# Kernel optimization log

Measured on AMD Instinct MI355X. Metric: run time of the kernel, lower is better.

## Reference

```python
import jax, jax.numpy as jnp
import numpy as np

D_MODEL = 1024
N_HEADS = 16
D_K = D_MODEL // N_HEADS


def setup_inputs() -> dict:
    key = jax.random.key(0)
    ks = jax.random.split(key, 12)
    B, S, D, H = 2, 2048, D_MODEL, N_HEADS
    s = 1.0 / np.sqrt(D)
    inp = {
        "x": jax.random.normal(ks[0], (B, S, D), jnp.float32),
        "Wq": jax.random.normal(ks[1], (D, D), jnp.float32) * s,
        "bq": jnp.zeros((D,), jnp.float32),
        "Wk": jax.random.normal(ks[2], (D, D), jnp.float32) * s,
        "bk": jnp.zeros((D,), jnp.float32),
        "Wv": jax.random.normal(ks[3], (D, D), jnp.float32) * s,
        "bv": jnp.zeros((D,), jnp.float32),
        "Wo": jax.random.normal(ks[4], (D, D), jnp.float32) * s,
        "bo": jnp.zeros((D,), jnp.float32),
        "Wp": jax.random.normal(ks[5], (D, H), jnp.float32) * s,
        "bp": jnp.zeros((H,), jnp.float32),
        "alpha": jax.random.normal(ks[6], (H,), jnp.float32) * 0.1,
    }
    return inp


def reference(x, Wq, bq, Wk, bk, Wv, bv, Wo, bo, Wp, bp, alpha):
    B, S, D = x.shape
    H, dk = N_HEADS, D_K
    scale = dk ** -0.5
    # projections -> (B, H, S, dk)
    Q = (x @ Wq + bq).reshape(B, S, H, dk).transpose(0, 2, 1, 3)
    K = (x @ Wk + bk).reshape(B, S, H, dk).transpose(0, 2, 1, 3)
    V = (x @ Wv + bv).reshape(B, S, H, dk).transpose(0, 2, 1, 3)
    scores = jnp.einsum("bhid,bhjd->bhij", Q, K) * scale  # (B,H,S,S)
    # phase derived from x: (B,S,H) -> (B,H,S)
    phase = (x @ Wp + bp).transpose(0, 2, 1)
    # coherence(i,j) = cos(phi_i - phi_j), per batch/head
    coherence = jnp.cos(phase[:, :, :, None] - phase[:, :, None, :])
    scores = scores + alpha[None, :, None, None] * coherence
    attn = jax.nn.softmax(scores, axis=-1)
    out = jnp.einsum("bhij,bhjd->bhid", attn, V)  # (B,H,S,dk)
    out = out.transpose(0, 2, 1, 3).reshape(B, S, D)
    return out @ Wo + bo
```

## Files before the change

kernel.cpp:

```cpp
#include <hip/hip_runtime.h>
#include <math.h>


#define S_LEN 2048
#define NHEADS 16

typedef __attribute__((ext_vector_type(8))) short short8;
typedef __attribute__((ext_vector_type(4))) float floatx4;
typedef __attribute__((ext_vector_type(4))) unsigned int uintx4;

__device__ inline unsigned short f2bf(float f) {
    union { float f; unsigned int i; } v; v.f = f;
    unsigned int u = v.i;
    return (unsigned short)((u + 0x7fffu + ((u >> 16) & 1u)) >> 16);
}
__device__ inline unsigned int pack2_bf16(float hi, float lo) {
    union { float f; unsigned int u; } a, b; a.f = hi; b.f = lo;
    return __builtin_amdgcn_perm(a.u, b.u, 0x07060302u);
}
__device__ inline void async_copy16(const unsigned short* src, unsigned short* dst_lds) {
    __builtin_amdgcn_global_load_lds(
        (const __attribute__((address_space(1))) unsigned int*)(src),
        (__attribute__((address_space(3))) unsigned int*)(dst_lds), 16, 0, 0);
}
__device__ inline void async_copy4(const float* src, float* dst_lds) {
    __builtin_amdgcn_global_load_lds(
        (const __attribute__((address_space(1))) unsigned int*)(src),
        (__attribute__((address_space(3))) unsigned int*)(dst_lds), 4, 0, 0);
}

__global__ __launch_bounds__(256) void prep_kernel(
    const float* __restrict__ x, const float* __restrict__ Wp,
    const float* __restrict__ bp,
    const float* __restrict__ w0, const float* __restrict__ w1,
    const float* __restrict__ w2, const float* __restrict__ w3,
    unsigned short* __restrict__ d0, unsigned short* __restrict__ d1,
    unsigned short* __restrict__ d2, unsigned short* __restrict__ d3,
    float* __restrict__ cosP, float* __restrict__ sinP,
    unsigned short* __restrict__ xb) {
    __shared__ __align__(16) unsigned short shmem[64 * 72];
    int t = threadIdx.x;
    if (blockIdx.x < 4096) {
        float* red = reinterpret_cast<float*>(shmem);
        int bid = blockIdx.x;
        int b = bid >> 11, s = bid & 2047;
        int h = t & 15, c = t >> 4;
        const float* xr = x + (size_t)bid * 1024;
        {
            float4 xv = *reinterpret_cast<const float4*>(&xr[t * 4]);
            uint2 o;
            o.x = (unsigned int)f2bf(xv.x) | ((unsigned int)f2bf(xv.y) << 16);
            o.y = (unsigned int)f2bf(xv.z) | ((unsigned int)f2bf(xv.w) << 16);
            *reinterpret_cast<uint2*>(&xb[(size_t)bid * 1024 + t * 4]) = o;
        }
        float acc = 0.f;
#pragma unroll 8
        for (int kk = 0; kk < 64; kk++) {
            int k = c * 64 + kk;
            acc += xr[k] * Wp[k * 16 + h];
        }
        red[t] = acc;
        __syncthreads();
        if (t < 16) {
            float sum = 0.f;
#pragma unroll
            for (int c2 = 0; c2 < 16; c2++) sum += red[c2 * 16 + t];
            sum += bp[t];
            float sv, cv;
            __sincosf(sum, &sv, &cv);
            size_t o = ((size_t)b * NHEADS + t) * S_LEN + s;
            cosP[o] = cv; sinP[o] = sv;
        }
    } else {
        unsigned short (*tile)[72] = reinterpret_cast<unsigned short (*)[72]>(shmem);
        int bid = blockIdx.x - 4096;
        int mat = bid >> 8;
        int tl  = bid & 255;
        int tr = tl >> 4, tc = tl & 15;
        const float* src    = (mat == 0) ? w0 : (mat == 1) ? w1 : (mat == 2) ? w2 : w3;
        unsigned short* dst = (mat == 0) ? d0 : (mat == 1) ? d1 : (mat == 2) ? d2 : d3;
        int col = t & 63, rbase = (t >> 6) * 16;
#pragma unroll
        for (int i = 0; i < 16; i++) {
            int row = rbase + i;
            tile[row][col] = f2bf(src[(size_t)(tr * 64 + row) * 1024 + tc * 64 + col]);
        }
        __syncthreads();
#pragma unroll
        for (int i = 0; i < 16; i++) {
            int row = rbase + i;
            dst[(size_t)(tc * 64 + row) * 1024 + tr * 64 + col] = tile[col][row];
        }
    }
}

template <int MT>
__global__ __launch_bounds__(256) void gemm_bt(
    const unsigned short* __restrict__ A, const unsigned short* __restrict__ BT,
    int N, int mode,
    const float* __restrict__ b0, const float* __restrict__ b1,
    const float* __restrict__ b2,
    unsigned short* __restrict__ o0, unsigned short* __restrict__ o1,
    unsigned short* __restrict__ o2, float* __restrict__ of) {
    __shared__ __align__(16) unsigned short As[MT * 32];
    __shared__ __align__(16) unsigned short Bs[128 * 32];
    const int K = 1024;
    const int MI = MT / 32;
    int t = threadIdx.x;
    int mBase = blockIdx.x * MT;
    int nBase = blockIdx.y * 128;
    int w = t >> 6, lane = t & 63, l15 = lane & 15, quad = lane >> 4;
    int wm = (w & 1) * (MT / 2), wn = (w >> 1) * 64;
    floatx4 acc[MI][4];
#pragma unroll
    for (int i = 0; i < MI; i++)
#pragma unroll
        for (int j = 0; j < 4; j++) acc[i][j] = (floatx4){0.f, 0.f, 0.f, 0.f};

    int arow = t >> 2, aseg = (t & 3) * 8;
    for (int k0 = 0; k0 < K; k0 += 32) {
        __syncthreads();
#pragma unroll
        for (int i = 0; i < MT / 64; i++)
            async_copy16(&A[(size_t)(mBase + i * 64 + arow) * K + k0 + aseg],
                         &As[(i * 64 + arow) * 32 + aseg]);
#pragma unroll
        for (int i = 0; i < 2; i++)
            async_copy16(&BT[(size_t)(nBase + i * 64 + arow) * K + k0 + aseg],
                         &Bs[(i * 64 + arow) * 32 + aseg]);
        __syncthreads();
        short8 af[MI], bfr[4];
#pragma unroll
        for (int mi = 0; mi < MI; mi++)
            af[mi] = *reinterpret_cast<const short8*>(&As[(wm + mi * 16 + l15) * 32 + quad * 8]);
#pragma unroll
        for (int ni = 0; ni < 4; ni++)
            bfr[ni] = *reinterpret_cast<const short8*>(&Bs[(wn + ni * 16 + l15) * 32 + quad * 8]);
#pragma unroll
        for (int mi = 0; mi < MI; mi++)
#pragma unroll
            for (int ni = 0; ni < 4; ni++)
                acc[mi][ni] = __builtin_amdgcn_mfma_f32_16x16x32_bf16(af[mi], bfr[ni], acc[mi][ni], 0, 0, 0);
    }

#pragma unroll
    for (int mi = 0; mi < MI; mi++) {
        int rowB = mBase + wm + mi * 16 + quad * 4;
#pragma unroll
        for (int ni = 0; ni < 4; ni++) {
            int col = nBase + wn + ni * 16 + l15;
            if (mode == 0) {
                float bias = b0[col];
#pragma unroll
                for (int r = 0; r < 4; r++) {
                    of[(size_t)(rowB + r) * N + col] = acc[mi][ni][r] + bias;
                }
            } else {
                int mat = col >> 10, nn = col & 1023;
                int h = nn >> 6, d = nn & 63;
                int b = rowB >> 11, sidx = rowB & 2047;
                if (mat == 2) {
                    float bv = b2[nn];
                    int jj = sidx & 63;
                    int a2 = jj >> 5, c2 = (jj >> 4) & 1, bb = jj & 15;
                    size_t rowOff = ((size_t)((b * NHEADS + h) * 64 + d)) * S_LEN +
                                    (sidx & ~63) + a2 * 32 + c2;
#pragma unroll
                    for (int r = 0; r < 4; r++)
                        o2[rowOff + 2 * (bb + r)] = f2bf(acc[mi][ni][r] + bv);
                } else {
                    const float* bias  = (mat == 0) ? b0 : b1;
                    unsigned short* op = (mat == 0) ? o0 : o1;
                    float bv = bias[nn];
                    float scl = (mat == 0) ? 0.18033688f : 1.0f;
#pragma unroll
                    for (int r = 0; r < 4; r++) {
                        float cv = (acc[mi][ni][r] + bv) * scl;
                        op[(((size_t)b * NHEADS + h) * S_LEN + (sidx + r)) * 64 + d] = f2bf(cv);
                    }
                }
            }
        }
    }
}

__global__ __launch_bounds__(512) void attn_kernel(
    const unsigned short* __restrict__ Qg, const unsigned short* __restrict__ Kg,
    const unsigned short* __restrict__ VTg,
    const float* __restrict__ cosP, const float* __restrict__ sinP,
    const float* __restrict__ alpha, unsigned short* __restrict__ ctx) {
    __shared__ __align__(16) unsigned short KsB[2][64 * 64];
    __shared__ __align__(16) unsigned short VtB[2][64 * 64];
    __shared__ __align__(16) float csB[2][128];
    __shared__ __align__(16) unsigned short Plb[8][16 * 72];

    int bid = blockIdx.x;
    int bh = bid >> 4, qt = bid & 15;
    int t = threadIdx.x, w = t >> 6, lane = t & 63, l15 = lane & 15, quad = lane >> 4;
    int m0 = qt * 128 + w * 16;
    size_t base = (size_t)bh * (S_LEN * 64);
    size_t phBase = (size_t)bh * S_LEN;
    const float L2E = 1.44269504f;

    int sj = t >> 3, sg = t & 7;
    int srot = ((sg - (sj & 7)) & 7) * 8;

    short8 qf[2];
#pragma unroll
    for (int c = 0; c < 2; c++)
        qf[c] = *reinterpret_cast<const short8*>(
            &Qg[base + (size_t)(m0 + l15) * 64 + c * 32 + quad * 8]);

    float alph = alpha[bh & 15] * L2E;
    float ci[4], si[4];
#pragma unroll
    for (int r = 0; r < 4; r++) {
        size_t o = phBase + m0 + quad * 4 + r;
        ci[r] = alph * cosP[o];
        si[r] = alph * sinP[o];
    }

    {
        async_copy16(&Kg[base + (size_t)sj * 64 + srot], &KsB[0][t * 8]);
        async_copy16(&VTg[base + (size_t)sj * S_LEN + srot], &VtB[0][t * 8]);
        if (w == 2)      async_copy4(&cosP[phBase + lane], &csB[0][lane]);
        else if (w == 3) async_copy4(&sinP[phBase + lane], &csB[0][64 + lane]);
    }

    floatx4 oacc[4], lacc;
#pragma unroll
    for (int tt = 0; tt < 4; tt++) oacc[tt] = (floatx4){0.f, 0.f, 0.f, 0.f};
    lacc = (floatx4){0.f, 0.f, 0.f, 0.f};
    const short8 ones8 = {(short)0x3F80, (short)0x3F80, (short)0x3F80, (short)0x3F80,
                          (short)0x3F80, (short)0x3F80, (short)0x3F80, (short)0x3F80};

    int rot = l15 & 7;
    int cb0 = 16 * ((quad + rot) & 7);
    int cb1 = 16 * ((quad + 4 + rot) & 7);

    for (int kt = 0; kt < 32; kt++) {
        int p = kt & 1;
        __syncthreads();
        if (kt < 31) {
            int kn = kt + 1, pn = p ^ 1;
            async_copy16(&Kg[base + (size_t)(kn * 64 + sj) * 64 + srot], &KsB[pn][t * 8]);
            async_copy16(&VTg[base + (size_t)sj * S_LEN + kn * 64 + srot], &VtB[pn][t * 8]);
            if (w == 2)      async_copy4(&cosP[phBase + kn * 64 + lane], &csB[pn][lane]);
            else if (w == 3) async_copy4(&sinP[phBase + kn * 64 + lane], &csB[pn][64 + lane]);
        }

        floatx4 st[4];
#pragma unroll
        for (int jt = 0; jt < 4; jt++) {
            const char* kr = (const char*)&KsB[p][(jt * 16 + l15) * 64];
            short8 kf0 = *reinterpret_cast<const short8*>(kr + cb0);
            short8 kf1 = *reinterpret_cast<const short8*>(kr + cb1);
            floatx4 s = (floatx4){0.f, 0.f, 0.f, 0.f};
            s = __builtin_amdgcn_mfma_f32_16x16x32_bf16(qf[0], kf0, s, 0, 0, 0);
            s = __builtin_amdgcn_mfma_f32_16x16x32_bf16(qf[1], kf1, s, 0, 0, 0);
            st[jt] = s;
        }

        float cjv[4], sjv[4];
#pragma unroll
        for (int jt = 0; jt < 4; jt++) {
            cjv[jt] = csB[p][jt * 16 + l15];
            sjv[jt] = csB[p][64 + jt * 16 + l15];
        }

        unsigned int* pl = reinterpret_cast<unsigned int*>(&Plb[w][0]);
#pragma unroll
        for (int r = 0; r < 4; r++) {
            float cc = ci[r], ss = si[r];
            float p0 = __builtin_amdgcn_exp2f(st[0][r] + cc * cjv[0] + ss * sjv[0]);
            float p1 = __builtin_amdgcn_exp2f(st[1][r] + cc * cjv[1] + ss * sjv[1]);
            float p2 = __builtin_amdgcn_exp2f(st[2][r] + cc * cjv[2] + ss * sjv[2]);
            float p3 = __builtin_amdgcn_exp2f(st[3][r] + cc * cjv[3] + ss * sjv[3]);
            int row = quad * 4 + r;
            pl[row * 36 + l15]      = pack2_bf16(p1, p0);
            pl[row * 36 + 16 + l15] = pack2_bf16(p3, p2);
        }

        short8 pf[2];
#pragma unroll
        for (int c = 0; c < 2; c++)
            pf[c] = *reinterpret_cast<const short8*>(
                &Plb[w][l15 * 72 + c * 32 + quad * 8]);

#pragma unroll
        for (int c = 0; c < 2; c++) {
            int cb = c ? cb1 : cb0;
#pragma unroll
            for (int tt = 0; tt < 4; tt++) {
                const char* vr = (const char*)&VtB[p][(tt * 16 + l15) * 64];
                short8 vf = *reinterpret_cast<const short8*>(vr + cb);
                oacc[tt] = __builtin_amdgcn_mfma_f32_16x16x32_bf16(pf[c], vf, oacc[tt], 0, 0, 0);
            }
            lacc = __builtin_amdgcn_mfma_f32_16x16x32_bf16(pf[c], ones8, lacc, 0, 0, 0);
        }
    }

    int b = bh >> 4, h = bh & 15;
    float inv[4];
#pragma unroll
    for (int r = 0; r < 4; r++) inv[r] = 1.0f / lacc[r];
#pragma unroll
    for (int tt = 0; tt < 4; tt++)
#pragma unroll
        for (int r = 0; r < 4; r++) {
            int srow = m0 + quad * 4 + r;
            ctx[((size_t)(b * S_LEN + srow)) * 1024 + h * 64 + tt * 16 + l15] =
                f2bf(oacc[tt][r] * inv[r]);
        }
}

extern "C" void kernel_launch(void* const* d_in, const int* in_sizes, int n_in,
                              void* d_out, int out_size, void* d_ws, size_t ws_size,
                              hipStream_t stream) {
    const float* x     = (const float*)d_in[0];
    const float* Wq    = (const float*)d_in[1];
    const float* bq    = (const float*)d_in[2];
    const float* Wk    = (const float*)d_in[3];
    const float* bk    = (const float*)d_in[4];
    const float* Wv    = (const float*)d_in[5];
    const float* bv    = (const float*)d_in[6];
    const float* Wo    = (const float*)d_in[7];
    const float* bo    = (const float*)d_in[8];
    const float* Wp    = (const float*)d_in[9];
    const float* bp    = (const float*)d_in[10];
    const float* alpha = (const float*)d_in[11];
    float* out = (float*)d_out;

    const size_t MB = 1048576;
    char* ws = (char*)d_ws;
    unsigned short* WT   = (unsigned short*)(ws);
    unsigned short* WoT  = (unsigned short*)(ws + 6 * MB);
    unsigned short* xb   = (unsigned short*)(ws + 8 * MB);
    unsigned short* ctx  = (unsigned short*)(ws + 8 * MB);
    unsigned short* Qw   = (unsigned short*)(ws + 16 * MB);
    unsigned short* Kw   = (unsigned short*)(ws + 24 * MB);
    unsigned short* VTg  = (unsigned short*)(ws + 32 * MB);
    float* cosP          = (float*)(ws + 40 * MB);
    float* sinP          = (float*)(ws + 40 * MB + 262144);

    prep_kernel<<<dim3(5120), dim3(256), 0, stream>>>(
        x, Wp, bp, Wq, Wk, Wv, Wo,
        WT, WT + 1048576, WT + 2097152, WoT, cosP, sinP, xb);
    gemm_bt<128><<<dim3(32, 24), dim3(256), 0, stream>>>(
        xb, WT, 3072, 1, bq, bk, bv, Qw, Kw, VTg, (float*)nullptr);
    attn_kernel<<<dim3(512), dim3(512), 0, stream>>>(
        Qw, Kw, VTg, cosP, sinP, alpha, ctx);
    gemm_bt<64><<<dim3(64, 8), dim3(256), 0, stream>>>(
        ctx, WoT, 1024, 0, bo, bo, bo,
        (unsigned short*)nullptr, (unsigned short*)nullptr,
        (unsigned short*)nullptr, out);
}
```

Baseline: 220.2 us.

## Enlarge attention blocks to 1024 threads, remap grid, pack phase math into float2

The attention kernel now runs 1024-thread blocks, each covering 256 query rows with 16 waves, so every staged K/V tile is reused by twice as many waves. The loading work is split so the first half of the threads copies K and the second half copies V^T. The block index is remapped so the 256 blocks spread batch-heads across consecutive block IDs. The coherence logit math is rewritten with float2 vectors so the compiler can emit packed FMAs. The trade-offs are a grid of only 256 blocks, which can under-fill the CUs, and heavier per-block barrier synchronisation.

```diff
diff --git a/kernel.cpp b/kernel.cpp
--- a/kernel.cpp
+++ b/kernel.cpp
@@ -7,6 +7,7 @@
 
 typedef __attribute__((ext_vector_type(8))) short short8;
 typedef __attribute__((ext_vector_type(4))) float floatx4;
+typedef __attribute__((ext_vector_type(2))) float float2v;
 typedef __attribute__((ext_vector_type(4))) unsigned int uintx4;
 
 __device__ inline unsigned short f2bf(float f) {
@@ -184,7 +185,7 @@
     }
 }
 
-__global__ __launch_bounds__(512) void attn_kernel(
+__global__ __launch_bounds__(1024) void attn_kernel(
     const unsigned short* __restrict__ Qg, const unsigned short* __restrict__ Kg,
     const unsigned short* __restrict__ VTg,
     const float* __restrict__ cosP, const float* __restrict__ sinP,
@@ -192,18 +193,21 @@
     __shared__ __align__(16) unsigned short KsB[2][64 * 64];
     __shared__ __align__(16) unsigned short VtB[2][64 * 64];
     __shared__ __align__(16) float csB[2][128];
-    __shared__ __align__(16) unsigned short Plb[8][16 * 72];
-
-    int bid = blockIdx.x;
-    int bh = bid >> 4, qt = bid & 15;
+    __shared__ __align__(16) unsigned short Plb[16][16 * 72];
+
+    int x = blockIdx.x;
+    int bh = (x & 7) * 4 + (x >> 6);
+    int qt = (x >> 3) & 7;
     int t = threadIdx.x, w = t >> 6, lane = t & 63, l15 = lane & 15, quad = lane >> 4;
-    int m0 = qt * 128 + w * 16;
+    int m0 = qt * 256 + w * 16;
     size_t base = (size_t)bh * (S_LEN * 64);
     size_t phBase = (size_t)bh * S_LEN;
     const float L2E = 1.44269504f;
 
-    int sj = t >> 3, sg = t & 7;
+    int th = t & 511;
+    int sj = th >> 3, sg = th & 7;
     int srot = ((sg - (sj & 7)) & 7) * 8;
+    bool stK = (t < 512);
 
     short8 qf[2];
 #pragma unroll
@@ -212,19 +216,19 @@
             &Qg[base + (size_t)(m0 + l15) * 64 + c * 32 + quad * 8]);
 
     float alph = alpha[bh & 15] * L2E;
-    float ci[4], si[4];
-#pragma unroll
-    for (int r = 0; r < 4; r++) {
-        size_t o = phBase + m0 + quad * 4 + r;
-        ci[r] = alph * cosP[o];
-        si[r] = alph * sinP[o];
+    float2v ci2[2], si2[2];
+#pragma unroll
+    for (int hh = 0; hh < 2; hh++) {
+        size_t o = phBase + m0 + quad * 4 + hh * 2;
+        ci2[hh] = (float2v){alph * cosP[o], alph * cosP[o + 1]};
+        si2[hh] = (float2v){alph * sinP[o], alph * sinP[o + 1]};
     }
 
     {
-        async_copy16(&Kg[base + (size_t)sj * 64 + srot], &KsB[0][t * 8]);
-        async_copy16(&VTg[base + (size_t)sj * S_LEN + srot], &VtB[0][t * 8]);
-        if (w == 2)      async_copy4(&cosP[phBase + lane], &csB[0][lane]);
-        else if (w == 3) async_copy4(&sinP[phBase + lane], &csB[0][64 + lane]);
+        if (stK) async_copy16(&Kg[base + (size_t)sj * 64 + srot], &KsB[0][th * 8]);
+        else     async_copy16(&VTg[base + (size_t)sj * S_LEN + srot], &VtB[0][th * 8]);
+        if (w == 4)      async_copy4(&cosP[phBase + lane], &csB[0][lane]);
+        else if (w == 5) async_copy4(&sinP[phBase + lane], &csB[0][64 + lane]);
     }
 
     floatx4 oacc[4], lacc;
@@ -243,10 +247,10 @@
         __syncthreads();
         if (kt < 31) {
             int kn = kt + 1, pn = p ^ 1;
-            async_copy16(&Kg[base + (size_t)(kn * 64 + sj) * 64 + srot], &KsB[pn][t * 8]);
-            async_copy16(&VTg[base + (size_t)sj * S_LEN + kn * 64 + srot], &VtB[pn][t * 8]);
-            if (w == 2)      async_copy4(&cosP[phBase + kn * 64 + lane], &csB[pn][lane]);
-            else if (w == 3) async_copy4(&sinP[phBase + kn * 64 + lane], &csB[pn][64 + lane]);
+            if (stK) async_copy16(&Kg[base + (size_t)(kn * 64 + sj) * 64 + srot], &KsB[pn][th * 8]);
+            else     async_copy16(&VTg[base + (size_t)sj * S_LEN + kn * 64 + srot], &VtB[pn][th * 8]);
+            if (w == 4)      async_copy4(&cosP[phBase + kn * 64 + lane], &csB[pn][lane]);
+            else if (w == 5) async_copy4(&sinP[phBase + kn * 64 + lane], &csB[pn][64 + lane]);
         }
 
         floatx4 st[4];
@@ -270,15 +274,27 @@
 
         unsigned int* pl = reinterpret_cast<unsigned int*>(&Plb[w][0]);
 #pragma unroll
-        for (int r = 0; r < 4; r++) {
-            float cc = ci[r], ss = si[r];
-            float p0 = __builtin_amdgcn_exp2f(st[0][r] + cc * cjv[0] + ss * sjv[0]);
-            float p1 = __builtin_amdgcn_exp2f(st[1][r] + cc * cjv[1] + ss * sjv[1]);
-            float p2 = __builtin_amdgcn_exp2f(st[2][r] + cc * cjv[2] + ss * sjv[2]);
-            float p3 = __builtin_amdgcn_exp2f(st[3][r] + cc * cjv[3] + ss * sjv[3]);
-            int row = quad * 4 + r;
-            pl[row * 36 + l15]      = pack2_bf16(p1, p0);
-            pl[row * 36 + 16 + l15] = pack2_bf16(p3, p2);
+        for (int rp = 0; rp < 2; rp++) {
+            float2v a0, a1, a2, a3;
+            {
+                float2v s0 = (float2v){st[0][rp * 2], st[0][rp * 2 + 1]};
+                float2v s1 = (float2v){st[1][rp * 2], st[1][rp * 2 + 1]};
+                float2v s2 = (float2v){st[2][rp * 2], st[2][rp * 2 + 1]};
+                float2v s3 = (float2v){st[3][rp * 2], st[3][rp * 2 + 1]};
+                a0 = si2[rp] * sjv[0] + (ci2[rp] * cjv[0] + s0);
+                a1 = si2[rp] * sjv[1] + (ci2[rp] * cjv[1] + s1);
+                a2 = si2[rp] * sjv[2] + (ci2[rp] * cjv[2] + s2);
+                a3 = si2[rp] * sjv[3] + (ci2[rp] * cjv[3] + s3);
+            }
+            int row = quad * 4 + rp * 2;
+            pl[row * 36 + l15]      = pack2_bf16(__builtin_amdgcn_exp2f(a1.x),
+                                                 __builtin_amdgcn_exp2f(a0.x));
+            pl[row * 36 + 16 + l15] = pack2_bf16(__builtin_amdgcn_exp2f(a3.x),
+                                                 __builtin_amdgcn_exp2f(a2.x));
+            pl[(row + 1) * 36 + l15]      = pack2_bf16(__builtin_amdgcn_exp2f(a1.y),
+                                                       __builtin_amdgcn_exp2f(a0.y));
+            pl[(row + 1) * 36 + 16 + l15] = pack2_bf16(__builtin_amdgcn_exp2f(a3.y),
+                                                       __builtin_amdgcn_exp2f(a2.y));
         }
 
         short8 pf[2];
@@ -348,7 +364,7 @@
         WT, WT + 1048576, WT + 2097152, WoT, cosP, sinP, xb);
     gemm_bt<128><<<dim3(32, 24), dim3(256), 0, stream>>>(
         xb, WT, 3072, 1, bq, bk, bv, Qw, Kw, VTg, (float*)nullptr);
-    attn_kernel<<<dim3(512), dim3(512), 0, stream>>>(
+    attn_kernel<<<dim3(256), dim3(1024), 0, stream>>>(
         Qw, Kw, VTg, cosP, sinP, alpha, ctx);
     gemm_bt<64><<<dim3(64, 8), dim3(256), 0, stream>>>(
         ctx, WoT, 1024, 0, bo, bo, bo,
```

After: 215.2 us. 2.3% less time.
